# Performance work log

Hardware: AMD Instinct MI355X
Metric: run time of the kernel (lower is better)

The kernel has to match this reference:

```python
import jax, jax.numpy as jnp
import numpy as np

B, I, T = 256, 64, 16
V, E, H = 4096, 256, 256


def setup_inputs() -> dict:
    key = jax.random.key(0)
    ks = jax.random.split(key, 12)
    emb = jax.random.normal(ks[0], (V, E), jnp.float32) * 0.02
    emb = emb.at[0].set(0.0)  # padding_idx=0
    s_e = 1.0 / np.sqrt(H)
    inp = {
        "batched_blocks": jax.random.randint(ks[1], (B, I, T), 0, V, jnp.int32),
        "actual_instr_counts": jax.random.randint(ks[2], (B,), 1, I + 1, jnp.int32),
        "actual_token_counts": jax.random.randint(ks[3], (B, I), 0, T + 1, jnp.int32),
        "embedding": emb,
        "Wih_tok": jax.random.uniform(ks[4], (4 * H, E), jnp.float32, -s_e, s_e),
        "Whh_tok": jax.random.uniform(ks[5], (4 * H, H), jnp.float32, -s_e, s_e),
        "b_tok": jax.random.uniform(ks[6], (4 * H,), jnp.float32, -s_e, s_e),
        "Wih_ins": jax.random.uniform(ks[7], (4 * H, H), jnp.float32, -s_e, s_e),
        "Whh_ins": jax.random.uniform(ks[8], (4 * H, H), jnp.float32, -s_e, s_e),
        "b_ins": jax.random.uniform(ks[9], (4 * H,), jnp.float32, -s_e, s_e),
        "linW": jax.random.uniform(ks[10], (1, H), jnp.float32, -s_e, s_e),
        "linb": jax.random.uniform(ks[11], (1,), jnp.float32, -s_e, s_e),
    }
    return inp


def _lstm_last(x, lengths, Wih, Whh, b):
    # x: [N, T, D]; returns hidden state at step lengths-1 (zeros if length==0),
    # matching pack_padded_sequence -> LSTM -> h_n semantics.
    N, Tt, _ = x.shape
    Hh = Whh.shape[1]

    def step(carry, xt):
        h, c = carry
        g = xt @ Wih.T + h @ Whh.T + b  # [N, 4H], torch gate order i,f,g,o
        i, f, gg, o = jnp.split(g, 4, axis=-1)
        c = jax.nn.sigmoid(f) * c + jax.nn.sigmoid(i) * jnp.tanh(gg)
        h = jax.nn.sigmoid(o) * jnp.tanh(c)
        return (h, c), h

    h0 = jnp.zeros((N, Hh), x.dtype)
    _, hs = jax.lax.scan(step, (h0, h0), jnp.swapaxes(x, 0, 1))  # [T, N, H]
    hs = jnp.swapaxes(hs, 0, 1)  # [N, T, H]
    idx = jnp.clip(lengths - 1, 0, Tt - 1).astype(jnp.int32)
    h_last = jnp.take_along_axis(hs, jnp.broadcast_to(idx[:, None, None], (N, 1, Hh)), axis=1)[:, 0]
    return jnp.where((lengths > 0)[:, None], h_last, jnp.zeros_like(h_last))


def reference(batched_blocks, actual_instr_counts, actual_token_counts,
              embedding, Wih_tok, Whh_tok, b_tok, Wih_ins, Whh_ins, b_ins,
              linW, linb):
    Bb, Ii, Tt = batched_blocks.shape
    tok_flat = batched_blocks.reshape(Bb * Ii, Tt)
    emb = embedding[tok_flat]  # [B*I, T, E]
    tok_len = actual_token_counts.reshape(-1)
    instr_repr = _lstm_last(emb, tok_len, Wih_tok, Whh_tok, b_tok)  # [B*I, H]
    instr_repr = instr_repr.reshape(Bb, Ii, -1)
    block_repr = _lstm_last(instr_repr, actual_instr_counts, Wih_ins, Whh_ins, b_ins)  # [B, H]
    return block_repr @ linW.T + linb  # [B, 1]
```

## Files before the change

kernel.cpp:

```cpp
#include <hip/hip_runtime.h>
#include <hip/hip_bf16.h>

#define Bq 256
#define Iq 64
#define Tq 16
#define Vq 4096
#define Eq 256
#define Hq 256
#define NSEQ 16384
#define HSTR 264
#define HR 272
#define HBUF 4352
#define CL 8
#define XCC_GETREG_IMM 6164

typedef __attribute__((ext_vector_type(8))) __bf16 bf16x8;
typedef __attribute__((ext_vector_type(8))) short short8;
typedef __attribute__((ext_vector_type(4))) float f32x4;

__device__ __forceinline__ bf16x8 as_bf8(short8 v) {
    union { short8 s; bf16x8 b; } u; u.s = v; return u.b;
}
__device__ __forceinline__ float sigf(float x) {
    return __builtin_amdgcn_rcpf(1.f + __expf(-x));
}
__device__ __forceinline__ float tanh_fast(float x) {
    float e = __expf(2.f * x);
    return 1.f - 2.f * __builtin_amdgcn_rcpf(e + 1.f);
}
__device__ __forceinline__ short bf16_rne(float x) {
    unsigned u = __float_as_uint(x);
    unsigned r = (u + 0x7fffu + ((u >> 16) & 1u)) >> 16;
    return (short)r;
}
__device__ __forceinline__ float bf16f(short h) {
    return __uint_as_float(((unsigned)(unsigned short)h) << 16);
}
__device__ __forceinline__ void gl_lds16(const unsigned* g, unsigned* l) {
    __builtin_amdgcn_global_load_lds(
        (const __attribute__((address_space(1))) void*)g,
        (__attribute__((address_space(3))) void*)l, 16, 0, 1);
}

__global__ void k_pack(const float* __restrict__ Wih_tok,
                       const float* __restrict__ b_tok,
                       const float* __restrict__ b_ins,
                       float* __restrict__ Wih4t,
                       float* __restrict__ b4t, float* __restrict__ b4i) {
    int g = blockIdx.x;
    int q = g >> 8;
    int j = g & 255;
    int k = threadIdx.x;
    Wih4t[(k * 256 + j) * 4 + q] = Wih_tok[g * Hq + k];
    if (k == 0) {
        b4t[j * 4 + q] = b_tok[g];
        b4i[j * 4 + q] = b_ins[g];
    }
}

__global__ void k_packB(const float* __restrict__ W0,
                        const float* __restrict__ W1,
                        short* __restrict__ B0h, short* __restrict__ B0l,
                        short* __restrict__ B1h, short* __restrict__ B1l) {
    int nt = blockIdx.x;
    int kc = blockIdx.y;
    int l  = threadIdx.x;
    int n = nt * 16 + (l & 15);
    int kb = kc * 32 + (l >> 4) * 8;
    size_t ob = ((size_t)(nt * 8 + kc) * 64 + l) * 8;
    #pragma unroll
    for (int m = 0; m < 8; ++m) {
        float v = W0[n * 256 + kb + m];
        short hi = bf16_rne(v);
        B0h[ob + m] = hi; B0l[ob + m] = bf16_rne(v - bf16f(hi));
        v = W1[n * 256 + kb + m];
        hi = bf16_rne(v);
        B1h[ob + m] = hi; B1l[ob + m] = bf16_rne(v - bf16f(hi));
    }
}

__global__ void k_packB2(const float* __restrict__ W2,
                         short* __restrict__ B2h, short* __restrict__ B2l) {
    int bx = blockIdx.x;
    int kc = blockIdx.y;
    int l  = threadIdx.x;
    int j  = bx >> 3, nt = bx & 7;
    int n_local = nt * 16 + (l & 15);
    int gate = n_local & 3;
    int u = j * 32 + (n_local >> 2);
    int row = gate * 256 + u;
    int kb = kc * 32 + (l >> 4) * 8;
    size_t ob = ((size_t)(bx * 8 + kc) * 64 + l) * 8;
    #pragma unroll
    for (int m = 0; m < 8; ++m) {
        float v = W2[row * 256 + kb + m];
        short hi = bf16_rne(v);
        B2h[ob + m] = hi;
        B2l[ob + m] = bf16_rne(v - bf16f(hi));
    }
}

__global__ __launch_bounds__(1024) void k_sortn(const int* __restrict__ len,
                                                int* __restrict__ perm,
                                                int n, int nbins) {
    __shared__ int cnt[65];
    __shared__ int base[65];
    int tid = threadIdx.x;
    if (tid < nbins) cnt[tid] = 0;
    __syncthreads();
    for (int i = tid; i < n; i += 1024) atomicAdd(&cnt[len[i]], 1);
    __syncthreads();
    if (tid == 0) {
        int acc = 0;
        for (int b = nbins - 1; b >= 0; --b) { base[b] = acc; acc += cnt[b]; }
    }
    __syncthreads();
    for (int i = tid; i < n; i += 1024) {
        int pos = atomicAdd(&base[len[i]], 1);
        perm[pos] = i;
    }
}

__global__ void k_zero(int* __restrict__ p, int n) {
    int i = blockIdx.x * blockDim.x + threadIdx.x;
    if (i < n) p[i] = 0;
}

__global__ __launch_bounds__(256) void k_epre(const float* __restrict__ emb,
                                              const float4* __restrict__ Wih4t,
                                              const float4* __restrict__ b4t,
                                              float4* __restrict__ Ep4) {
    __shared__ float es[8][Eq];
    int tid = threadIdx.x;
    int v0 = blockIdx.x * 8;
    #pragma unroll
    for (int r = 0; r < 8; ++r) es[r][tid] = emb[(v0 + r) * Eq + tid];
    __syncthreads();
    float4 a[8];
    #pragma unroll
    for (int r = 0; r < 8; ++r) a[r] = make_float4(0.f, 0.f, 0.f, 0.f);
    const float4* Wp = Wih4t + tid;
    #pragma unroll 2
    for (int k = 0; k < Eq; ++k) {
        float4 wv = Wp[k * 256];
        #pragma unroll
        for (int r = 0; r < 8; ++r) {
            float e = es[r][k];
            a[r].x += wv.x * e; a[r].y += wv.y * e;
            a[r].z += wv.z * e; a[r].w += wv.w * e;
        }
    }
    float4 b4 = b4t[tid];
    #pragma unroll
    for (int r = 0; r < 8; ++r) {
        Ep4[(size_t)(v0 + r) * 256 + tid] =
            make_float4(a[r].x + b4.x, a[r].y + b4.y, a[r].z + b4.z, a[r].w + b4.w);
    }
}

#define MFMA_KC_BODY(BH, BL) { \
    bf16x8 ahi = *(const bf16x8*)(hc0 + kc * 32 + quad * 8); \
    bf16x8 alo = *(const bf16x8*)(hc1 + kc * 32 + quad * 8); \
    const short* bhb = (BH) + (size_t)(w * 4 * 8 + kc) * 512 + lane * 8; \
    const short* blb = (BL) + (size_t)(w * 4 * 8 + kc) * 512 + lane * 8; \
    _Pragma("unroll") \
    for (int g = 0; g < 4; ++g) { \
        _Pragma("unroll") \
        for (int q = 0; q < 4; ++q) { \
            bf16x8 bh = *(const bf16x8*)(bhb + g * 65536 + q * 4096); \
            bf16x8 bl = *(const bf16x8*)(blb + g * 65536 + q * 4096); \
            acc[g][q] = __builtin_amdgcn_mfma_f32_16x16x32_bf16(ahi, bh, acc[g][q], 0, 0, 0); \
            acc[g][q] = __builtin_amdgcn_mfma_f32_16x16x32_bf16(alo, bh, acc[g][q], 0, 0, 0); \
            acc[g][q] = __builtin_amdgcn_mfma_f32_16x16x32_bf16(ahi, bl, acc[g][q], 0, 0, 0); \
        } \
    } }

__global__ __launch_bounds__(256) void k_token_mfma(
        const int* __restrict__ tokens,
        const int* __restrict__ tok_len,
        const int* __restrict__ perm,
        const float4* __restrict__ Ep4,
        const short* __restrict__ Bhi, const short* __restrict__ Blo,
        const short* __restrict__ BXhi, const short* __restrict__ BXlo,
        const float4* __restrict__ b4i,
        float4* __restrict__ Xp4) {
    __shared__ __align__(16) short hb[2][2][16 * HSTR];
    __shared__ int toks[16][Tq];
    __shared__ int lens[16];
    __shared__ int sid[16];
    int tid  = threadIdx.x;
    int w    = tid >> 6;
    int lane = tid & 63;
    int l15  = lane & 15;
    int quad = lane >> 4;
    int s0   = blockIdx.x * 16;

    if (tid < 16) {
        int q = perm[s0 + tid];
        sid[tid]  = q;
        lens[tid] = tok_len[q];
    }
    {
        int* hz = (int*)&hb[0][0][0];
        for (int i = tid; i < 16 * HSTR; i += 256) hz[i] = 0;
    }
    __syncthreads();
    toks[tid >> 4][tid & 15] = tokens[sid[tid >> 4] * Tq + (tid & 15)];
    int lenr[4];
    #pragma unroll
    for (int r = 0; r < 4; ++r) lenr[r] = lens[quad * 4 + r];
    int tmax = 0;
    #pragma unroll
    for (int s = 0; s < 16; ++s) tmax = max(tmax, lens[s]);
    __syncthreads();

    f32x4 acc[4][4];
    float cst[4][4], hst[4][4];
    #pragma unroll
    for (int q = 0; q < 4; ++q)
        #pragma unroll
        for (int r = 0; r < 4; ++r) { cst[q][r] = 0.f; hst[q][r] = 0.f; }
    int ubase = w * 64;

    for (int t = 0; t < tmax; ++t) {
        #pragma unroll
        for (int q = 0; q < 4; ++q) {
            int u = ubase + q * 16 + l15;
            #pragma unroll
            for (int r = 0; r < 4; ++r) {
                float4 e = Ep4[(size_t)toks[quad * 4 + r][t] * 256 + u];
                acc[0][q][r] = e.x; acc[1][q][r] = e.y;
                acc[2][q][r] = e.z; acc[3][q][r] = e.w;
            }
        }
        const short* hc0 = &hb[t & 1][0][l15 * HSTR];
        const short* hc1 = &hb[t & 1][1][l15 * HSTR];
        #pragma unroll 1
        for (int kc = 0; kc < 8; ++kc) MFMA_KC_BODY(Bhi, Blo)
        short* hn0 = &hb[(t + 1) & 1][0][0];
        short* hn1 = &hb[(t + 1) & 1][1][0];
        #pragma unroll
        for (int q = 0; q < 4; ++q) {
            int u = ubase + q * 16 + l15;
            #pragma unroll
            for (int r = 0; r < 4; ++r) {
                int s = quad * 4 + r;
                if (t < lenr[r]) {
                    float cn = sigf(acc[1][q][r]) * cst[q][r]
                             + sigf(acc[0][q][r]) * tanh_fast(acc[2][q][r]);
                    cst[q][r] = cn;
                    hst[q][r] = sigf(acc[3][q][r]) * tanh_fast(cn);
                }
                float hv = hst[q][r];
                short hi = bf16_rne(hv);
                hn0[s * HSTR + u] = hi;
                hn1[s * HSTR + u] = bf16_rne(hv - bf16f(hi));
            }
        }
        __syncthreads();
    }

    #pragma unroll
    for (int q = 0; q < 4; ++q) {
        float4 bb = b4i[ubase + q * 16 + l15];
        #pragma unroll
        for (int r = 0; r < 4; ++r) {
            acc[0][q][r] = bb.x; acc[1][q][r] = bb.y;
            acc[2][q][r] = bb.z; acc[3][q][r] = bb.w;
        }
    }
    {
        const short* hc0 = &hb[tmax & 1][0][l15 * HSTR];
        const short* hc1 = &hb[tmax & 1][1][l15 * HSTR];
        #pragma unroll 1
        for (int kc = 0; kc < 8; ++kc) MFMA_KC_BODY(BXhi, BXlo)
    }
    #pragma unroll
    for (int q = 0; q < 4; ++q) {
        int u = ubase + q * 16 + l15;
        #pragma unroll
        for (int r = 0; r < 4; ++r) {
            Xp4[(size_t)sid[quad * 4 + r] * 256 + u] =
                make_float4(acc[0][q][r], acc[1][q][r], acc[2][q][r], acc[3][q][r]);
        }
    }
}

__global__ __launch_bounds__(256) void k_instr_xcd(
        const float* __restrict__ XpF,
        const int* __restrict__ instr_cnt,
        const int* __restrict__ perm2,
        const short* __restrict__ B2h, const short* __restrict__ B2l,
        int* __restrict__ xcd_cnt,
        int* __restrict__ flags,
        unsigned* __restrict__ hG,
        const float* __restrict__ linW,
        const float* __restrict__ linb,
        float* __restrict__ out) {
    __shared__ __align__(16) short Bs[2][32768];
    __shared__ __align__(16) unsigned hS[HBUF];
    __shared__ int lens[16], sid[16], role[2];
    int tid  = threadIdx.x;
    int w    = tid >> 6;
    int lane = tid & 63;
    int l15  = lane & 15;
    int quad = lane >> 4;

    if (tid == 0) {
        int xcd = __builtin_amdgcn_s_getreg(XCC_GETREG_IMM) & 7;
        int slot = atomicAdd(&xcd_cnt[xcd], 1);
        role[0] = xcd; role[1] = slot;
    }
    __syncthreads();
    int slot = role[1];
    if (slot >= 16) return;
    int c = role[0] * 2 + (slot >> 3);
    int j = slot & 7;

    if (tid < 16) {
        int q = perm2[c * 16 + tid];
        sid[tid]  = q;
        lens[tid] = instr_cnt[q];
    }
    {
        const float4* s0 = (const float4*)(B2h + (size_t)j * 32768);
        const float4* s1 = (const float4*)(B2l + (size_t)j * 32768);
        float4* d0 = (float4*)&Bs[0][0];
        float4* d1 = (float4*)&Bs[1][0];
        for (int i = tid; i < 4096; i += 256) { d0[i] = s0[i]; d1[i] = s1[i]; }
    }
    __syncthreads();
    int tmax = 0;
    #pragma unroll
    for (int s = 0; s < 16; ++s) tmax = max(tmax, lens[s]);
    int lenr[4], sidr[4];
    #pragma unroll
    for (int r = 0; r < 4; ++r) { lenr[r] = lens[quad * 4 + r]; sidr[r] = sid[quad * 4 + r]; }

    float cst[2][4], hst[2][4];
    #pragma unroll
    for (int r = 0; r < 4; ++r) { cst[0][r] = cst[1][r] = 0.f; hst[0][r] = hst[1][r] = 0.f; }
    int T0 = 2 * w, T1 = 2 * w + 1;
    unsigned* hGc = hG + (size_t)c * (4 * HBUF);
    int* flg = flags + c * 65 * 8;
    int gbase = l15 & ~3;

    for (int t = 0; t < tmax; ++t) {
        f32x4 acc0, acc1;
        #pragma unroll
        for (int r = 0; r < 4; ++r) {
            size_t base = ((size_t)sidr[r] * Iq + t) * 1024 + j * 128;
            acc0[r] = XpF[base + T0 * 16 + l15];
            acc1[r] = XpF[base + T1 * 16 + l15];
        }
        if (t > 0) {
            const volatile int* fp = flg + (t - 1) * 8;
            int cap = 0;
            while (true) {
                int ok = (lane < 8) ? (fp[lane] != 0) : 1;
                if (__all(ok)) break;
                if (++cap > (1 << 22)) break;
                __builtin_amdgcn_s_sleep(1);
            }
        }
        {
            const unsigned* hRdG = hGc + (size_t)(t & 3) * HBUF;
            #pragma unroll
            for (int rr = 0; rr < 4; ++rr)
                gl_lds16(hRdG + (rr * 256 + tid) * 4, hS + (rr * 256 + tid) * 4);
            if (tid < 64) gl_lds16(hRdG + (1024 + tid) * 4, hS + (1024 + tid) * 4);
        }
        __syncthreads();
        const unsigned* hrow = hS + l15 * HR;
        #pragma unroll
        for (int kc = 0; kc < 8; ++kc) {
            unsigned hp[8];
            *(uint4*)&hp[0] = *(const uint4*)(hrow + kc * 32 + quad * 8);
            *(uint4*)&hp[4] = *(const uint4*)(hrow + kc * 32 + quad * 8 + 4);
            short8 vhi, vlo;
            #pragma unroll
            for (int m = 0; m < 8; ++m) {
                vhi[m] = (short)(hp[m] & 0xffffu);
                vlo[m] = (short)(hp[m] >> 16);
            }
            bf16x8 ahi = as_bf8(vhi), alo = as_bf8(vlo);
            bf16x8 bh0 = *(const bf16x8*)(&Bs[0][((T0 * 8 + kc) * 64 + lane) * 8]);
            bf16x8 bl0 = *(const bf16x8*)(&Bs[1][((T0 * 8 + kc) * 64 + lane) * 8]);
            bf16x8 bh1 = *(const bf16x8*)(&Bs[0][((T1 * 8 + kc) * 64 + lane) * 8]);
            bf16x8 bl1 = *(const bf16x8*)(&Bs[1][((T1 * 8 + kc) * 64 + lane) * 8]);
            acc0 = __builtin_amdgcn_mfma_f32_16x16x32_bf16(ahi, bh0, acc0, 0, 0, 0);
            acc0 = __builtin_amdgcn_mfma_f32_16x16x32_bf16(alo, bh0, acc0, 0, 0, 0);
            acc0 = __builtin_amdgcn_mfma_f32_16x16x32_bf16(ahi, bl0, acc0, 0, 0, 0);
            acc1 = __builtin_amdgcn_mfma_f32_16x16x32_bf16(ahi, bh1, acc1, 0, 0, 0);
            acc1 = __builtin_amdgcn_mfma_f32_16x16x32_bf16(alo, bh1, acc1, 0, 0, 0);
            acc1 = __builtin_amdgcn_mfma_f32_16x16x32_bf16(ahi, bl1, acc1, 0, 0, 0);
        }
        unsigned* hWr = hGc + (size_t)((t + 1) & 3) * HBUF;
        #pragma unroll
        for (int r = 0; r < 4; ++r) {
            float v0 = acc0[r], v1 = acc1[r];
            float gi0 = __shfl(v0, gbase + 0, 16), gf0 = __shfl(v0, gbase + 1, 16);
            float gg0 = __shfl(v0, gbase + 2, 16), go0 = __shfl(v0, gbase + 3, 16);
            float gi1 = __shfl(v1, gbase + 0, 16), gf1 = __shfl(v1, gbase + 1, 16);
            float gg1 = __shfl(v1, gbase + 2, 16), go1 = __shfl(v1, gbase + 3, 16);
            if (t < lenr[r]) {
                float cn0 = sigf(gf0) * cst[0][r] + sigf(gi0) * tanh_fast(gg0);
                cst[0][r] = cn0;
                hst[0][r] = sigf(go0) * tanh_fast(cn0);
                float cn1 = sigf(gf1) * cst[1][r] + sigf(gi1) * tanh_fast(gg1);
                cst[1][r] = cn1;
                hst[1][r] = sigf(go1) * tanh_fast(cn1);
            }
        }
        if ((l15 & 3) == 0) {
            int u0 = 32 * j + 4 * T0 + (l15 >> 2);
            int u1 = 32 * j + 4 * T1 + (l15 >> 2);
            #pragma unroll
            for (int r = 0; r < 4; ++r) {
                int s = quad * 4 + r;
                float h0 = hst[0][r], h1 = hst[1][r];
                short h0h = bf16_rne(h0), h1h = bf16_rne(h1);
                unsigned p0 = (unsigned)(unsigned short)h0h |
                              ((unsigned)(unsigned short)bf16_rne(h0 - bf16f(h0h)) << 16);
                unsigned p1 = (unsigned)(unsigned short)h1h |
                              ((unsigned)(unsigned short)bf16_rne(h1 - bf16f(h1h)) << 16);
                hWr[s * HR + u0] = p0;
                hWr[s * HR + u1] = p1;
            }
        }
        __syncthreads();
        if (tid == 0) *(volatile int*)(flg + t * 8 + j) = 1;
    }

    if (j == 0) {
        const volatile int* fp = flg + (tmax - 1) * 8;
        int cap = 0;
        while (true) {
            int ok = (lane < 8) ? (fp[lane] != 0) : 1;
            if (__all(ok)) break;
            if (++cap > (1 << 22)) break;
            __builtin_amdgcn_s_sleep(1);
        }
        const unsigned* hRdG = hGc + (size_t)(tmax & 3) * HBUF;
        #pragma unroll
        for (int rr = 0; rr < 4; ++rr)
            gl_lds16(hRdG + (rr * 256 + tid) * 4, hS + (rr * 256 + tid) * 4);
        if (tid < 64) gl_lds16(hRdG + (1024 + tid) * 4, hS + (1024 + tid) * 4);
        __syncthreads();
        int s = tid >> 4, k0 = (tid & 15) * 16;
        float p = 0.f;
        #pragma unroll
        for (int m = 0; m < 16; ++m) {
            int u = k0 + m;
            unsigned pk = hS[s * HR + u];
            float hv = bf16f((short)(pk & 0xffffu)) + bf16f((short)(pk >> 16));
            p += linW[u] * hv;
        }
        p += __shfl_down(p, 8, 16);
        p += __shfl_down(p, 4, 16);
        p += __shfl_down(p, 2, 16);
        p += __shfl_down(p, 1, 16);
        if ((tid & 15) == 0) out[sid[s]] = p + linb[0];
    }
}

extern "C" void kernel_launch(void* const* d_in, const int* in_sizes, int n_in,
                              void* d_out, int out_size, void* d_ws, size_t ws_size,
                              hipStream_t stream) {
    const int*   tokens  = (const int*)d_in[0];
    const int*   icnt    = (const int*)d_in[1];
    const int*   tcnt    = (const int*)d_in[2];
    const float* emb     = (const float*)d_in[3];
    const float* Wih_tok = (const float*)d_in[4];
    const float* Whh_tok = (const float*)d_in[5];
    const float* b_tok   = (const float*)d_in[6];
    const float* Wih_ins = (const float*)d_in[7];
    const float* Whh_ins = (const float*)d_in[8];
    const float* b_ins   = (const float*)d_in[9];
    const float* linW    = (const float*)d_in[10];
    const float* linb    = (const float*)d_in[11];
    float* out = (float*)d_out;

    float* ws_f    = (float*)d_ws;
    float* Wih4t   = ws_f;
    float* b4t     = Wih4t + 262144;
    float* b4i     = b4t + 1024;
    int*   perm    = (int*)(b4i + 1024);
    int*   perm2   = perm + 16384;
    int*   xcd_cnt = perm2 + 256;
    int*   flags   = xcd_cnt + 8;
    int*   sync_end= flags + 8320;
    short* Bhi     = (short*)(sync_end + 376);
    short* Blo     = Bhi + 262144;
    short* BXhi    = Blo + 262144;
    short* BXlo    = BXhi + 262144;
    short* B2h     = BXlo + 262144;
    short* B2l     = B2h + 262144;
    unsigned* hG   = (unsigned*)(B2l + 262144);
    float* Ep4     = (float*)(hG + 278528);
    float* Xp4     = Ep4 + 4194304;

    size_t need = ((char*)(Xp4 + 16777216)) - ((char*)d_ws);
    if (ws_size < need) return;

    hipLaunchKernelGGL(k_pack, dim3(1024), dim3(256), 0, stream,
                       Wih_tok, b_tok, b_ins, Wih4t, b4t, b4i);
    hipLaunchKernelGGL(k_packB, dim3(64, 8), dim3(64), 0, stream,
                       Whh_tok, Wih_ins, Bhi, Blo, BXhi, BXlo);
    hipLaunchKernelGGL(k_packB2, dim3(64, 8), dim3(64), 0, stream,
                       Whh_ins, B2h, B2l);
    hipLaunchKernelGGL(k_sortn, dim3(1), dim3(1024), 0, stream, tcnt, perm, NSEQ, 17);
    hipLaunchKernelGGL(k_sortn, dim3(1), dim3(1024), 0, stream, icnt, perm2, Bq, 65);
    hipLaunchKernelGGL(k_zero, dim3(33), dim3(256), 0, stream, xcd_cnt, 8328);
    hipLaunchKernelGGL(k_zero, dim3(1088), dim3(256), 0, stream, (int*)hG, 278528);
    hipLaunchKernelGGL(k_epre, dim3(512), dim3(256), 0, stream,
                       emb, (const float4*)Wih4t, (const float4*)b4t, (float4*)Ep4);
    hipLaunchKernelGGL(k_token_mfma, dim3(1024), dim3(256), 0, stream,
                       tokens, tcnt, perm, (const float4*)Ep4,
                       Bhi, Blo, BXhi, BXlo, (const float4*)b4i, (float4*)Xp4);
    hipLaunchKernelGGL(k_instr_xcd, dim3(256), dim3(256), 0, stream,
                       Xp4, icnt, perm2, B2h, B2l, xcd_cnt, flags, hG,
                       linW, linb, out);
}
```

Measured before the change: 918.9 us.

## Process 32 sequences per block with 512 threads to reuse weight loads

The token LSTM kernel now handles 32 sequences per workgroup instead of 16, using 8 waves of 512 threads. Each wave covers two 16-unit hidden slices across two 16-row M tiles, so every B-fragment load of Whh/Wih_ins feeds two MFMA tiles instead of one. This halves global weight traffic per sequence. The cost is that a block now runs to the longest length among 32 sorted sequences, more shared memory per block, and more accumulator registers per thread.

```diff
diff --git a/kernel.cpp b/kernel.cpp
--- a/kernel.cpp
+++ b/kernel.cpp
@@ -158,24 +158,12 @@
     }
 }
 
-#define MFMA_KC_BODY(BH, BL) { \
-    bf16x8 ahi = *(const bf16x8*)(hc0 + kc * 32 + quad * 8); \
-    bf16x8 alo = *(const bf16x8*)(hc1 + kc * 32 + quad * 8); \
-    const short* bhb = (BH) + (size_t)(w * 4 * 8 + kc) * 512 + lane * 8; \
-    const short* blb = (BL) + (size_t)(w * 4 * 8 + kc) * 512 + lane * 8; \
-    _Pragma("unroll") \
-    for (int g = 0; g < 4; ++g) { \
-        _Pragma("unroll") \
-        for (int q = 0; q < 4; ++q) { \
-            bf16x8 bh = *(const bf16x8*)(bhb + g * 65536 + q * 4096); \
-            bf16x8 bl = *(const bf16x8*)(blb + g * 65536 + q * 4096); \
-            acc[g][q] = __builtin_amdgcn_mfma_f32_16x16x32_bf16(ahi, bh, acc[g][q], 0, 0, 0); \
-            acc[g][q] = __builtin_amdgcn_mfma_f32_16x16x32_bf16(alo, bh, acc[g][q], 0, 0, 0); \
-            acc[g][q] = __builtin_amdgcn_mfma_f32_16x16x32_bf16(ahi, bl, acc[g][q], 0, 0, 0); \
-        } \
-    } }
-
-__global__ __launch_bounds__(256) void k_token_mfma(
+#define MFMA3(accv, ah, al, bh, bl) \
+    accv = __builtin_amdgcn_mfma_f32_16x16x32_bf16(ah, bh, accv, 0, 0, 0); \
+    accv = __builtin_amdgcn_mfma_f32_16x16x32_bf16(al, bh, accv, 0, 0, 0); \
+    accv = __builtin_amdgcn_mfma_f32_16x16x32_bf16(ah, bl, accv, 0, 0, 0);
+
+__global__ __launch_bounds__(512) void k_token_mfma(
         const int* __restrict__ tokens,
         const int* __restrict__ tok_len,
         const int* __restrict__ perm,
@@ -184,105 +172,150 @@
         const short* __restrict__ BXhi, const short* __restrict__ BXlo,
         const float4* __restrict__ b4i,
         float4* __restrict__ Xp4) {
-    __shared__ __align__(16) short hb[2][2][16 * HSTR];
-    __shared__ int toks[16][Tq];
-    __shared__ int lens[16];
-    __shared__ int sid[16];
+    __shared__ __align__(16) short hb[2][2][32 * HSTR];
+    __shared__ int toks[32][Tq];
+    __shared__ int lens[32];
+    __shared__ int sid[32];
     int tid  = threadIdx.x;
     int w    = tid >> 6;
     int lane = tid & 63;
     int l15  = lane & 15;
     int quad = lane >> 4;
-    int s0   = blockIdx.x * 16;
-
-    if (tid < 16) {
+    int s0   = blockIdx.x * 32;
+
+    if (tid < 32) {
         int q = perm[s0 + tid];
         sid[tid]  = q;
         lens[tid] = tok_len[q];
     }
     {
         int* hz = (int*)&hb[0][0][0];
-        for (int i = tid; i < 16 * HSTR; i += 256) hz[i] = 0;
+        for (int i = tid; i < 32 * HSTR; i += 512) hz[i] = 0;
     }
     __syncthreads();
     toks[tid >> 4][tid & 15] = tokens[sid[tid >> 4] * Tq + (tid & 15)];
-    int lenr[4];
-    #pragma unroll
-    for (int r = 0; r < 4; ++r) lenr[r] = lens[quad * 4 + r];
+    int lenr[2][4], sidr[2][4];
+    #pragma unroll
+    for (int mt = 0; mt < 2; ++mt)
+        #pragma unroll
+        for (int r = 0; r < 4; ++r) {
+            lenr[mt][r] = lens[mt * 16 + quad * 4 + r];
+            sidr[mt][r] = sid[mt * 16 + quad * 4 + r];
+        }
     int tmax = 0;
     #pragma unroll
-    for (int s = 0; s < 16; ++s) tmax = max(tmax, lens[s]);
-    __syncthreads();
-
-    f32x4 acc[4][4];
-    float cst[4][4], hst[4][4];
-    #pragma unroll
-    for (int q = 0; q < 4; ++q)
-        #pragma unroll
-        for (int r = 0; r < 4; ++r) { cst[q][r] = 0.f; hst[q][r] = 0.f; }
-    int ubase = w * 64;
+    for (int s = 0; s < 32; ++s) tmax = max(tmax, lens[s]);
+    __syncthreads();
+
+    f32x4 acc[2][4][2];
+    float cst[2][2][4], hst[2][2][4];
+    #pragma unroll
+    for (int u2 = 0; u2 < 2; ++u2)
+        #pragma unroll
+        for (int mt = 0; mt < 2; ++mt)
+            #pragma unroll
+            for (int r = 0; r < 4; ++r) { cst[u2][mt][r] = 0.f; hst[u2][mt][r] = 0.f; }
 
     for (int t = 0; t < tmax; ++t) {
         #pragma unroll
-        for (int q = 0; q < 4; ++q) {
-            int u = ubase + q * 16 + l15;
-            #pragma unroll
-            for (int r = 0; r < 4; ++r) {
-                float4 e = Ep4[(size_t)toks[quad * 4 + r][t] * 256 + u];
-                acc[0][q][r] = e.x; acc[1][q][r] = e.y;
-                acc[2][q][r] = e.z; acc[3][q][r] = e.w;
-            }
-        }
-        const short* hc0 = &hb[t & 1][0][l15 * HSTR];
-        const short* hc1 = &hb[t & 1][1][l15 * HSTR];
+        for (int u2 = 0; u2 < 2; ++u2) {
+            int u = (w + u2 * 8) * 16 + l15;
+            #pragma unroll
+            for (int mt = 0; mt < 2; ++mt)
+                #pragma unroll
+                for (int r = 0; r < 4; ++r) {
+                    float4 e = Ep4[(size_t)toks[mt * 16 + quad * 4 + r][t] * 256 + u];
+                    acc[u2][0][mt][r] = e.x; acc[u2][1][mt][r] = e.y;
+                    acc[u2][2][mt][r] = e.z; acc[u2][3][mt][r] = e.w;
+                }
+        }
+        const short* hc0 = &hb[t & 1][0][0];
+        const short* hc1 = &hb[t & 1][1][0];
         #pragma unroll 1
-        for (int kc = 0; kc < 8; ++kc) MFMA_KC_BODY(Bhi, Blo)
+        for (int kc = 0; kc < 8; ++kc) {
+            bf16x8 a0h = *(const bf16x8*)(hc0 + l15 * HSTR + kc * 32 + quad * 8);
+            bf16x8 a0l = *(const bf16x8*)(hc1 + l15 * HSTR + kc * 32 + quad * 8);
+            bf16x8 a1h = *(const bf16x8*)(hc0 + (16 + l15) * HSTR + kc * 32 + quad * 8);
+            bf16x8 a1l = *(const bf16x8*)(hc1 + (16 + l15) * HSTR + kc * 32 + quad * 8);
+            #pragma unroll
+            for (int u2 = 0; u2 < 2; ++u2)
+                #pragma unroll
+                for (int g = 0; g < 4; ++g) {
+                    size_t bo = ((size_t)((g * 16 + w + u2 * 8) * 8 + kc)) * 512 + lane * 8;
+                    bf16x8 bh = *(const bf16x8*)(Bhi + bo);
+                    bf16x8 bl = *(const bf16x8*)(Blo + bo);
+                    MFMA3(acc[u2][g][0], a0h, a0l, bh, bl)
+                    MFMA3(acc[u2][g][1], a1h, a1l, bh, bl)
+                }
+        }
         short* hn0 = &hb[(t + 1) & 1][0][0];
         short* hn1 = &hb[(t + 1) & 1][1][0];
         #pragma unroll
-        for (int q = 0; q < 4; ++q) {
-            int u = ubase + q * 16 + l15;
+        for (int u2 = 0; u2 < 2; ++u2) {
+            int u = (w + u2 * 8) * 16 + l15;
+            #pragma unroll
+            for (int mt = 0; mt < 2; ++mt)
+                #pragma unroll
+                for (int r = 0; r < 4; ++r) {
+                    int s = mt * 16 + quad * 4 + r;
+                    if (t < lenr[mt][r]) {
+                        float cn = sigf(acc[u2][1][mt][r]) * cst[u2][mt][r]
+                                 + sigf(acc[u2][0][mt][r]) * tanh_fast(acc[u2][2][mt][r]);
+                        cst[u2][mt][r] = cn;
+                        hst[u2][mt][r] = sigf(acc[u2][3][mt][r]) * tanh_fast(cn);
+                    }
+                    float hv = hst[u2][mt][r];
+                    short hi = bf16_rne(hv);
+                    hn0[s * HSTR + u] = hi;
+                    hn1[s * HSTR + u] = bf16_rne(hv - bf16f(hi));
+                }
+        }
+        __syncthreads();
+    }
+
+    #pragma unroll
+    for (int u2 = 0; u2 < 2; ++u2) {
+        float4 bb = b4i[(w + u2 * 8) * 16 + l15];
+        #pragma unroll
+        for (int mt = 0; mt < 2; ++mt)
             #pragma unroll
             for (int r = 0; r < 4; ++r) {
-                int s = quad * 4 + r;
-                if (t < lenr[r]) {
-                    float cn = sigf(acc[1][q][r]) * cst[q][r]
-                             + sigf(acc[0][q][r]) * tanh_fast(acc[2][q][r]);
-                    cst[q][r] = cn;
-                    hst[q][r] = sigf(acc[3][q][r]) * tanh_fast(cn);
+                acc[u2][0][mt][r] = bb.x; acc[u2][1][mt][r] = bb.y;
+                acc[u2][2][mt][r] = bb.z; acc[u2][3][mt][r] = bb.w;
+            }
+    }
+    {
+        const short* hc0 = &hb[tmax & 1][0][0];
+        const short* hc1 = &hb[tmax & 1][1][0];
+        #pragma unroll 1
+        for (int kc = 0; kc < 8; ++kc) {
+            bf16x8 a0h = *(const bf16x8*)(hc0 + l15 * HSTR + kc * 32 + quad * 8);
+            bf16x8 a0l = *(const bf16x8*)(hc1 + l15 * HSTR + kc * 32 + quad * 8);
+            bf16x8 a1h = *(const bf16x8*)(hc0 + (16 + l15) * HSTR + kc * 32 + quad * 8);
+            bf16x8 a1l = *(const bf16x8*)(hc1 + (16 + l15) * HSTR + kc * 32 + quad * 8);
+            #pragma unroll
+            for (int u2 = 0; u2 < 2; ++u2)
+                #pragma unroll
+                for (int g = 0; g < 4; ++g) {
+                    size_t bo = ((size_t)((g * 16 + w + u2 * 8) * 8 + kc)) * 512 + lane * 8;
+                    bf16x8 bh = *(const bf16x8*)(BXhi + bo);
+                    bf16x8 bl = *(const bf16x8*)(BXlo + bo);
+                    MFMA3(acc[u2][g][0], a0h, a0l, bh, bl)
+                    MFMA3(acc[u2][g][1], a1h, a1l, bh, bl)
                 }
-                float hv = hst[q][r];
-                short hi = bf16_rne(hv);
-                hn0[s * HSTR + u] = hi;
-                hn1[s * HSTR + u] = bf16_rne(hv - bf16f(hi));
+        }
+    }
+    #pragma unroll
+    for (int u2 = 0; u2 < 2; ++u2) {
+        int u = (w + u2 * 8) * 16 + l15;
+        #pragma unroll
+        for (int mt = 0; mt < 2; ++mt)
+            #pragma unroll
+            for (int r = 0; r < 4; ++r) {
+                Xp4[(size_t)sidr[mt][r] * 256 + u] =
+                    make_float4(acc[u2][0][mt][r], acc[u2][1][mt][r],
+                                acc[u2][2][mt][r], acc[u2][3][mt][r]);
             }
-        }
-        __syncthreads();
-    }
-
-    #pragma unroll
-    for (int q = 0; q < 4; ++q) {
-        float4 bb = b4i[ubase + q * 16 + l15];
-        #pragma unroll
-        for (int r = 0; r < 4; ++r) {
-            acc[0][q][r] = bb.x; acc[1][q][r] = bb.y;
-            acc[2][q][r] = bb.z; acc[3][q][r] = bb.w;
-        }
-    }
-    {
-        const short* hc0 = &hb[tmax & 1][0][l15 * HSTR];
-        const short* hc1 = &hb[tmax & 1][1][l15 * HSTR];
-        #pragma unroll 1
-        for (int kc = 0; kc < 8; ++kc) MFMA_KC_BODY(BXhi, BXlo)
-    }
-    #pragma unroll
-    for (int q = 0; q < 4; ++q) {
-        int u = ubase + q * 16 + l15;
-        #pragma unroll
-        for (int r = 0; r < 4; ++r) {
-            Xp4[(size_t)sid[quad * 4 + r] * 256 + u] =
-                make_float4(acc[0][q][r], acc[1][q][r], acc[2][q][r], acc[3][q][r]);
-        }
     }
 }
 
@@ -515,7 +548,7 @@
     hipLaunchKernelGGL(k_zero, dim3(1088), dim3(256), 0, stream, (int*)hG, 278528);
     hipLaunchKernelGGL(k_epre, dim3(512), dim3(256), 0, stream,
                        emb, (const float4*)Wih4t, (const float4*)b4t, (float4*)Ep4);
-    hipLaunchKernelGGL(k_token_mfma, dim3(1024), dim3(256), 0, stream,
+    hipLaunchKernelGGL(k_token_mfma, dim3(512), dim3(512), 0, stream,
                        tokens, tcnt, perm, (const float4*)Ep4,
                        Bhi, Blo, BXhi, BXlo, (const float4*)b4i, (float4*)Xp4);
     hipLaunchKernelGGL(k_instr_xcd, dim3(256), dim3(256), 0, stream,
```

After: 803.6 us. 1.14x faster.
